# Kernel optimization log

Measured on AMD Instinct MI355X. Metric: run time of the kernel, lower is better.

## Reference

```python
import jax, jax.numpy as jnp
import numpy as np
import math

H = 8  # num_heads

def setup_inputs() -> dict:
    key = jax.random.key(0)
    ks = jax.random.split(key, 12)
    B, N, M, k = 2, 8192, 8192, 32
    dq, dk, dv = 256, 256, 256
    s = 1.0 / math.sqrt(dq)
    inp = {
        'Q': jax.random.normal(ks[0], (B, N, dq), dtype=jnp.float32),
        'K': jax.random.normal(ks[1], (B, M, dk), dtype=jnp.float32),
        'neighbours': jax.random.randint(ks[2], (B, N, k), 0, M),
        'Wq': jax.random.normal(ks[3], (dq, dv), dtype=jnp.float32) * s,
        'bq': jnp.zeros((dv,), dtype=jnp.float32),
        'Wk': jax.random.normal(ks[4], (dk, dv), dtype=jnp.float32) * s,
        'bk': jnp.zeros((dv,), dtype=jnp.float32),
        'Wv': jax.random.normal(ks[5], (dk, dv), dtype=jnp.float32) * s,
        'bv': jnp.zeros((dv,), dtype=jnp.float32),
        'Wo': jax.random.normal(ks[6], (dv, dv), dtype=jnp.float32) * (1.0 / math.sqrt(dv)),
        'bo': jnp.zeros((dv,), dtype=jnp.float32),
    }
    return inp

def reference(Q, K, neighbours, Wq, bq, Wk, bk, Wv, bv, Wo, bo):
    B, N, _ = Q.shape
    dv = Wq.shape[1]
    ds = dv // H
    # project and split heads (contiguous channel chunks == reshape)
    Qh = (Q @ Wq + bq).reshape(B, N, H, ds)            # [B,N,H,ds]
    Kh = (K @ Wk + bk).reshape(B, -1, H, ds)           # [B,M,H,ds]
    Vh = (K @ Wv + bv).reshape(B, -1, H, ds)           # [B,M,H,ds]
    # gather per-node kNN neighbour keys/values: [B,N,k,H,ds]
    gather = jax.vmap(lambda x, idx: x[idx])
    Kn = gather(Kh, neighbours)
    Vn = gather(Vh, neighbours)
    # scale uses full latent size (faithful to original), not head dim
    scale = 1.0 / math.sqrt(dv)
    E = jnp.einsum('bnhd,bnkhd->bnhk', Qh, Kn) * scale  # [B,N,H,k]
    A = jax.nn.softmax(E, axis=-1)
    AV = jnp.einsum('bnhk,bnkhd->bnhd', A, Vn).reshape(B, N, dv)
    return AV @ Wo + bo
```

## Files before the change

### kernel.cpp

```cpp
#include <hip/hip_runtime.h>
#include <stdint.h>

typedef unsigned short u16;
typedef __attribute__((ext_vector_type(8))) short short8;
typedef __attribute__((ext_vector_type(4))) float f32x4;

__device__ __forceinline__ float bf2f(u16 u) {
    union { unsigned int i; float f; } v;
    v.i = ((unsigned int)u) << 16;
    return v.f;
}
__device__ __forceinline__ u16 f2bf(float f) {
    union { float f; unsigned int i; } v; v.f = f;
    unsigned int b = v.i;
    return (u16)((b + 0x7FFFu + ((b >> 16) & 1u)) >> 16);
}

typedef const __attribute__((address_space(1))) void* as1cv;
typedef __attribute__((address_space(3))) void* as3v;
__device__ __forceinline__ void gload16(const void* g, void* l) {
    __builtin_amdgcn_global_load_lds((as1cv)g, (as3v)l, 16, 0, 0);
}

__global__ __launch_bounds__(256) void prep(
    const float* __restrict__ Q, const float* __restrict__ K,
    const float* __restrict__ Wq, const float* __restrict__ Wk,
    const float* __restrict__ Wv, const float* __restrict__ Wo,
    u16* __restrict__ Qb, u16* __restrict__ Kb,
    u16* __restrict__ Tq, u16* __restrict__ Tk,
    u16* __restrict__ Tv, u16* __restrict__ To)
{
    __shared__ u16 ts[64][65];
    int bi = blockIdx.x;
    int t = threadIdx.x;
    if (bi < 4096) {
        const float* src = (bi < 2048) ? Q : K;
        u16* dst = (bi < 2048) ? Qb : Kb;
        int blk = bi & 2047;
        size_t i = ((size_t)blk * 256 + t) * 8;
        float4 a = *reinterpret_cast<const float4*>(src + i);
        float4 b = *reinterpret_cast<const float4*>(src + i + 4);
        u16 o[8] = {f2bf(a.x), f2bf(a.y), f2bf(a.z), f2bf(a.w),
                    f2bf(b.x), f2bf(b.y), f2bf(b.z), f2bf(b.w)};
        *reinterpret_cast<uint4*>(dst + i) = *reinterpret_cast<const uint4*>(o);
        return;
    }
    int wi = bi - 4096;
    int wsel = wi >> 4;
    const float* W = wsel == 0 ? Wq : wsel == 1 ? Wk : wsel == 2 ? Wv : Wo;
    u16*        T  = wsel == 0 ? Tq : wsel == 1 ? Tk : wsel == 2 ? Tv : To;
    int k0 = ((wi >> 2) & 3) * 64, n0 = (wi & 3) * 64;
    int r = t >> 2, cq = (t & 3) * 16;
    const float4* src = reinterpret_cast<const float4*>(W + (k0 + r) * 256 + n0 + cq);
    for (int u = 0; u < 4; ++u) {
        float4 v = src[u];
        int c = cq + u * 4;
        ts[r][c + 0] = f2bf(v.x); ts[r][c + 1] = f2bf(v.y);
        ts[r][c + 2] = f2bf(v.z); ts[r][c + 3] = f2bf(v.w);
    }
    __syncthreads();
    u16* dst = T + (n0 + r) * 256 + k0 + cq;
    for (int u = 0; u < 16; ++u) dst[u] = ts[cq + u][r];
}

__global__ __launch_bounds__(256) void gemm_proj(
    const u16* __restrict__ Qb, const u16* __restrict__ Kb,
    const u16* __restrict__ Wtq, const u16* __restrict__ Wtk, const u16* __restrict__ Wtv,
    const float* __restrict__ bq, const float* __restrict__ bk, const float* __restrict__ bv,
    u16* __restrict__ Qh, u16* __restrict__ Kh, u16* __restrict__ Vh)
{
    int z = blockIdx.z;
    const u16*   Ab   = (z == 0) ? Qb  : Kb;
    const u16*   Wt   = (z == 0) ? Wtq : (z == 1) ? Wtk : Wtv;
    const float* bias = (z == 0) ? bq  : (z == 1) ? bk  : bv;
    u16*         C    = (z == 0) ? Qh  : (z == 1) ? Kh  : Vh;

    __shared__ u16 As[64 * 64];
    __shared__ u16 Bs[128 * 64];

    int t = threadIdx.x;
    int lane = t & 63, w = t >> 6;
    int row0 = blockIdx.x * 64, col0 = blockIdx.y * 128;
    int wr = (w >> 1) * 32, wc = (w & 1) * 64;
    int qd = lane >> 4, md = lane & 15;

    int lrow = lane >> 3;
    int scol = (lane & 7) * 8;

    f32x4 acc[2][4] = {};

    for (int kt = 0; kt < 256; kt += 64) {
#pragma unroll
        for (int u = 0; u < 2; ++u) {
            int ch = w * 2 + u;
            gload16(Ab + (size_t)(row0 + ch * 8 + lrow) * 256 + kt + scol,
                    (char*)As + ch * 1024);
        }
#pragma unroll
        for (int u = 0; u < 4; ++u) {
            int ch = w * 4 + u;
            gload16(Wt + (size_t)(col0 + ch * 8 + lrow) * 256 + kt + scol,
                    (char*)Bs + ch * 1024);
        }
        __syncthreads();
#pragma unroll
        for (int ks = 0; ks < 64; ks += 32) {
            short8 af[2], bf[4];
#pragma unroll
            for (int i = 0; i < 2; ++i)
                af[i] = *reinterpret_cast<const short8*>(
                    &As[(wr + i * 16 + md) * 64 + ks + qd * 8]);
#pragma unroll
            for (int j = 0; j < 4; ++j)
                bf[j] = *reinterpret_cast<const short8*>(
                    &Bs[(wc + j * 16 + md) * 64 + ks + qd * 8]);
#pragma unroll
            for (int i = 0; i < 2; ++i)
#pragma unroll
                for (int j = 0; j < 4; ++j)
                    acc[i][j] = __builtin_amdgcn_mfma_f32_16x16x32_bf16(
                        af[i], bf[j], acc[i][j], 0, 0, 0);
        }
        __syncthreads();
    }

#pragma unroll
    for (int i = 0; i < 2; ++i)
#pragma unroll
        for (int j = 0; j < 4; ++j) {
            int col = col0 + wc + j * 16 + md;
            float b = bias[col];
#pragma unroll
            for (int r = 0; r < 4; ++r) {
                int row = row0 + wr + i * 16 + qd * 4 + r;
                C[(size_t)row * 256 + col] = f2bf(acc[i][j][r] + b);
            }
        }
}

__global__ __launch_bounds__(256) void gemm_out(
    const u16* __restrict__ Ab, const u16* __restrict__ Wt,
    const float* __restrict__ bias, float* __restrict__ Cout)
{
    __shared__ u16 As[64 * 64];
    __shared__ u16 Bs[64 * 64];

    int t = threadIdx.x;
    int lane = t & 63, w = t >> 6;
    int row0 = blockIdx.x * 64, col0 = blockIdx.y * 64;
    int wr = (w >> 1) * 32, wc = (w & 1) * 32;
    int qd = lane >> 4, md = lane & 15;

    int lrow = lane >> 3;
    int scol = (lane & 7) * 8;

    f32x4 acc[2][2] = {};

    for (int kt = 0; kt < 256; kt += 64) {
#pragma unroll
        for (int u = 0; u < 2; ++u) {
            int ch = w * 2 + u;
            gload16(Ab + (size_t)(row0 + ch * 8 + lrow) * 256 + kt + scol,
                    (char*)As + ch * 1024);
            gload16(Wt + (size_t)(col0 + ch * 8 + lrow) * 256 + kt + scol,
                    (char*)Bs + ch * 1024);
        }
        __syncthreads();
#pragma unroll
        for (int ks = 0; ks < 64; ks += 32) {
            short8 af[2], bf[2];
#pragma unroll
            for (int i = 0; i < 2; ++i)
                af[i] = *reinterpret_cast<const short8*>(
                    &As[(wr + i * 16 + md) * 64 + ks + qd * 8]);
#pragma unroll
            for (int j = 0; j < 2; ++j)
                bf[j] = *reinterpret_cast<const short8*>(
                    &Bs[(wc + j * 16 + md) * 64 + ks + qd * 8]);
#pragma unroll
            for (int i = 0; i < 2; ++i)
#pragma unroll
                for (int j = 0; j < 2; ++j)
                    acc[i][j] = __builtin_amdgcn_mfma_f32_16x16x32_bf16(
                        af[i], bf[j], acc[i][j], 0, 0, 0);
        }
        __syncthreads();
    }

#pragma unroll
    for (int i = 0; i < 2; ++i)
#pragma unroll
        for (int j = 0; j < 2; ++j) {
            int col = col0 + wc + j * 16 + md;
            float b = bias[col];
#pragma unroll
            for (int r = 0; r < 4; ++r) {
                int row = row0 + wr + i * 16 + qd * 4 + r;
                Cout[(size_t)row * 256 + col] = acc[i][j][r] + b;
            }
        }
}

__global__ __launch_bounds__(256) void attn(
    const u16* __restrict__ Qh, const u16* __restrict__ Kh, const u16* __restrict__ Vh,
    const int* __restrict__ nbr, u16* __restrict__ AVb)
{
    __shared__ float qs[2][256];
    __shared__ float as_[2][256];
    __shared__ int jb[2][32];

    int t = threadIdx.x;
    int row0 = blockIdx.x * 2;
    int b = row0 >> 13;

    {
        int r = t >> 7, c = (t & 127) * 2;
        unsigned int v = *reinterpret_cast<const unsigned int*>(
            Qh + (size_t)(row0 + r) * 256 + c);
        union { unsigned int i; float f; } lo, hi;
        lo.i = v << 16; hi.i = v & 0xffff0000u;
        qs[r][c] = lo.f; qs[r][c + 1] = hi.f;
    }
    if (t < 64) {
        int r = t >> 5, j = t & 31;
        int ji = nbr[(size_t)(row0 + r) * 32 + j];
        jb[r][j] = ((b << 13) + ji) << 9;
    }
    __syncthreads();

    int h = t >> 5, j = t & 31;
#pragma unroll
    for (int r = 0; r < 2; ++r) {
        const char* kp = (const char*)Kh + jb[r][j] + h * 64;
        uint4 kw[4];
        kw[0] = *reinterpret_cast<const uint4*>(kp);
        kw[1] = *reinterpret_cast<const uint4*>(kp + 16);
        kw[2] = *reinterpret_cast<const uint4*>(kp + 32);
        kw[3] = *reinterpret_cast<const uint4*>(kp + 48);
        const float* q = &qs[r][h * 32];
        float e = 0.f;
#pragma unroll
        for (int cq4 = 0; cq4 < 4; ++cq4) {
            unsigned int wds[4] = {kw[cq4].x, kw[cq4].y, kw[cq4].z, kw[cq4].w};
#pragma unroll
            for (int u = 0; u < 4; ++u) {
                union { unsigned int i; float f; } lo, hi;
                lo.i = wds[u] << 16; hi.i = wds[u] & 0xffff0000u;
                e += q[cq4 * 8 + u * 2] * lo.f + q[cq4 * 8 + u * 2 + 1] * hi.f;
            }
        }
        e *= 0.0625f;
        float m = e;
        for (int off = 16; off; off >>= 1) m = fmaxf(m, __shfl_xor(m, off, 32));
        float p = __expf(e - m);
        float s = p;
        for (int off = 16; off; off >>= 1) s += __shfl_xor(s, off, 32);
        as_[r][t] = p / s;
    }
    __syncthreads();

    {
        int r = t >> 7, c = t & 127, hh = c >> 4;
        const float* aw = &as_[r][hh * 32];
        float a0 = 0.f, a1 = 0.f;
#pragma unroll
        for (int jj = 0; jj < 32; ++jj) {
            unsigned int v = *reinterpret_cast<const unsigned int*>(
                (const char*)Vh + jb[r][jj] + c * 4);
            union { unsigned int i; float f; } lo, hi;
            lo.i = v << 16; hi.i = v & 0xffff0000u;
            float wgt = aw[jj];
            a0 += wgt * lo.f; a1 += wgt * hi.f;
        }
        u16 o[2] = {f2bf(a0), f2bf(a1)};
        *reinterpret_cast<unsigned int*>(AVb + (size_t)(row0 + r) * 256 + c * 2) =
            *reinterpret_cast<const unsigned int*>(o);
    }
}

extern "C" void kernel_launch(void* const* d_in, const int* in_sizes, int n_in,
                              void* d_out, int out_size, void* d_ws, size_t ws_size,
                              hipStream_t stream) {
    const float* Q   = (const float*)d_in[0];
    const float* K   = (const float*)d_in[1];
    const int*   nbr = (const int*)d_in[2];
    const float* Wq  = (const float*)d_in[3];
    const float* bq  = (const float*)d_in[4];
    const float* Wk  = (const float*)d_in[5];
    const float* bk  = (const float*)d_in[6];
    const float* Wv  = (const float*)d_in[7];
    const float* bv  = (const float*)d_in[8];
    const float* Wo  = (const float*)d_in[9];
    const float* bo  = (const float*)d_in[10];
    float* out = (float*)d_out;

    char* ws = (char*)d_ws;
    size_t off = 0;
    auto alloc = [&](size_t bytes) -> void* {
        void* p = ws + off;
        off += (bytes + 255) & ~(size_t)255;
        return p;
    };
    const size_t MN = 16384;
    u16* Wtq = (u16*)alloc(256 * 256 * 2);
    u16* Wtk = (u16*)alloc(256 * 256 * 2);
    u16* Wtv = (u16*)alloc(256 * 256 * 2);
    u16* Wto = (u16*)alloc(256 * 256 * 2);
    u16* Qb  = (u16*)alloc(MN * 256 * 2);
    u16* Kb  = (u16*)alloc(MN * 256 * 2);
    u16* Qh  = (u16*)alloc(MN * 256 * 2);
    u16* Kh  = (u16*)alloc(MN * 256 * 2);
    u16* Vh  = (u16*)alloc(MN * 256 * 2);
    u16* AVb = (u16*)alloc(MN * 256 * 2);

    prep<<<dim3(4160), 256, 0, stream>>>(Q, K, Wq, Wk, Wv, Wo,
                                         Qb, Kb, Wtq, Wtk, Wtv, Wto);
    gemm_proj<<<dim3(256, 2, 3), 256, 0, stream>>>(Qb, Kb, Wtq, Wtk, Wtv,
                                                   bq, bk, bv, Qh, Kh, Vh);
    attn<<<dim3(8192), 256, 0, stream>>>(Qh, Kh, Vh, nbr, AVb);
    gemm_out<<<dim3(256, 4), 256, 0, stream>>>(AVb, Wto, bo, out);
}
```

Baseline: 170.8 us.

## Fuse fp32-to-bf16 input conversion into projection GEMM and retile kernels

Removes the separate Q/K fp32-to-bf16 conversion pass. The projection GEMM now loads fp32 tiles directly into LDS with an XOR swizzle and converts them to bf16 in registers, using 128x128 tiles. The output GEMM moves to 64x128 tiles with swizzled LDS, and the attention kernel handles 4 rows per block, using vectorized V loads and readfirstlane offsets. This cuts a full HBM round trip for Q and K, at the cost of larger LDS use (48KB) and more conversion work inside the GEMM loop.

```diff
diff --git a/kernel.cpp b/kernel.cpp
--- a/kernel.cpp
+++ b/kernel.cpp
@@ -1,55 +1,43 @@
 #include <hip/hip_runtime.h>
+#include <hip/hip_bf16.h>
 #include <stdint.h>
 
 typedef unsigned short u16;
 typedef __attribute__((ext_vector_type(8))) short short8;
 typedef __attribute__((ext_vector_type(4))) float f32x4;
 
-__device__ __forceinline__ float bf2f(u16 u) {
-    union { unsigned int i; float f; } v;
-    v.i = ((unsigned int)u) << 16;
-    return v.f;
-}
 __device__ __forceinline__ u16 f2bf(float f) {
     union { float f; unsigned int i; } v; v.f = f;
     unsigned int b = v.i;
     return (u16)((b + 0x7FFFu + ((b >> 16) & 1u)) >> 16);
 }
 
+__device__ __forceinline__ short8 cvt8(float4 a, float4 b) {
+    union { __hip_bfloat162 h[4]; short8 s; } u;
+    u.h[0] = __float22bfloat162_rn(make_float2(a.x, a.y));
+    u.h[1] = __float22bfloat162_rn(make_float2(a.z, a.w));
+    u.h[2] = __float22bfloat162_rn(make_float2(b.x, b.y));
+    u.h[3] = __float22bfloat162_rn(make_float2(b.z, b.w));
+    return u.s;
+}
+
 typedef const __attribute__((address_space(1))) void* as1cv;
 typedef __attribute__((address_space(3))) void* as3v;
 __device__ __forceinline__ void gload16(const void* g, void* l) {
     __builtin_amdgcn_global_load_lds((as1cv)g, (as3v)l, 16, 0, 0);
 }
 
-__global__ __launch_bounds__(256) void prep(
-    const float* __restrict__ Q, const float* __restrict__ K,
-    const float* __restrict__ Wq, const float* __restrict__ Wk,
-    const float* __restrict__ Wv, const float* __restrict__ Wo,
-    u16* __restrict__ Qb, u16* __restrict__ Kb,
-    u16* __restrict__ Tq, u16* __restrict__ Tk,
-    u16* __restrict__ Tv, u16* __restrict__ To)
+__global__ __launch_bounds__(256) void wprep(
+    const float* __restrict__ W0, const float* __restrict__ W1,
+    const float* __restrict__ W2, const float* __restrict__ W3,
+    u16* __restrict__ T0, u16* __restrict__ T1,
+    u16* __restrict__ T2, u16* __restrict__ T3)
 {
+    const float* W = blockIdx.z == 0 ? W0 : blockIdx.z == 1 ? W1 : blockIdx.z == 2 ? W2 : W3;
+    u16*        T  = blockIdx.z == 0 ? T0 : blockIdx.z == 1 ? T1 : blockIdx.z == 2 ? T2 : T3;
     __shared__ u16 ts[64][65];
-    int bi = blockIdx.x;
+    int k0 = blockIdx.x * 64, n0 = blockIdx.y * 64;
     int t = threadIdx.x;
-    if (bi < 4096) {
-        const float* src = (bi < 2048) ? Q : K;
-        u16* dst = (bi < 2048) ? Qb : Kb;
-        int blk = bi & 2047;
-        size_t i = ((size_t)blk * 256 + t) * 8;
-        float4 a = *reinterpret_cast<const float4*>(src + i);
-        float4 b = *reinterpret_cast<const float4*>(src + i + 4);
-        u16 o[8] = {f2bf(a.x), f2bf(a.y), f2bf(a.z), f2bf(a.w),
-                    f2bf(b.x), f2bf(b.y), f2bf(b.z), f2bf(b.w)};
-        *reinterpret_cast<uint4*>(dst + i) = *reinterpret_cast<const uint4*>(o);
-        return;
-    }
-    int wi = bi - 4096;
-    int wsel = wi >> 4;
-    const float* W = wsel == 0 ? Wq : wsel == 1 ? Wk : wsel == 2 ? Wv : Wo;
-    u16*        T  = wsel == 0 ? Tq : wsel == 1 ? Tk : wsel == 2 ? Tv : To;
-    int k0 = ((wi >> 2) & 3) * 64, n0 = (wi & 3) * 64;
     int r = t >> 2, cq = (t & 3) * 16;
     const float4* src = reinterpret_cast<const float4*>(W + (k0 + r) * 256 + n0 + cq);
     for (int u = 0; u < 4; ++u) {
@@ -64,17 +52,92 @@
 }
 
 __global__ __launch_bounds__(256) void gemm_proj(
-    const u16* __restrict__ Qb, const u16* __restrict__ Kb,
+    const float* __restrict__ Q, const float* __restrict__ K,
     const u16* __restrict__ Wtq, const u16* __restrict__ Wtk, const u16* __restrict__ Wtv,
     const float* __restrict__ bq, const float* __restrict__ bk, const float* __restrict__ bv,
     u16* __restrict__ Qh, u16* __restrict__ Kh, u16* __restrict__ Vh)
 {
     int z = blockIdx.z;
-    const u16*   Ab   = (z == 0) ? Qb  : Kb;
+    const float* Af   = (z == 0) ? Q   : K;
     const u16*   Wt   = (z == 0) ? Wtq : (z == 1) ? Wtk : Wtv;
     const float* bias = (z == 0) ? bq  : (z == 1) ? bk  : bv;
     u16*         C    = (z == 0) ? Qh  : (z == 1) ? Kh  : Vh;
 
+    __shared__ float Asf[128 * 64];
+    __shared__ u16   Bs[128 * 64];
+
+    int t = threadIdx.x;
+    int lane = t & 63, w = t >> 6;
+    int row0 = blockIdx.x * 128, col0 = blockIdx.y * 128;
+    int wr = (w >> 1) * 64, wc = (w & 1) * 64;
+    int qd = lane >> 4, md = lane & 15;
+
+    f32x4 acc[4][4] = {};
+
+    for (int kt = 0; kt < 256; kt += 64) {
+#pragma unroll
+        for (int u = 0; u < 8; ++u) {
+            int chunk = w * 8 + u;
+            int s = chunk * 64 + lane;
+            int r = s >> 4, c = s & 15;
+            gload16(Af + (size_t)(row0 + r) * 256 + kt + ((c ^ (r & 15)) * 4),
+                    (char*)Asf + chunk * 1024);
+        }
+#pragma unroll
+        for (int u = 0; u < 4; ++u) {
+            int chunk = w * 4 + u;
+            int s = chunk * 64 + lane;
+            int r = s >> 3, c = s & 7;
+            gload16(Wt + (size_t)(col0 + r) * 256 + kt + ((c ^ (r & 7)) * 8),
+                    (char*)Bs + chunk * 1024);
+        }
+        __syncthreads();
+#pragma unroll
+        for (int ks = 0; ks < 64; ks += 32) {
+            short8 af[4], bf[4];
+#pragma unroll
+            for (int i = 0; i < 4; ++i) {
+                int ar = wr + i * 16 + md;
+                int c0 = (ks >> 2) + qd * 2;
+                int x = ar & 15;
+                float4 fa0 = reinterpret_cast<const float4*>(Asf)[ar * 16 + (c0 ^ x)];
+                float4 fa1 = reinterpret_cast<const float4*>(Asf)[ar * 16 + ((c0 + 1) ^ x)];
+                af[i] = cvt8(fa0, fa1);
+            }
+#pragma unroll
+            for (int j = 0; j < 4; ++j) {
+                int br = wc + j * 16 + md;
+                int slot = ((ks >> 3) + qd) ^ (br & 7);
+                bf[j] = reinterpret_cast<const short8*>(Bs)[br * 8 + slot];
+            }
+#pragma unroll
+            for (int i = 0; i < 4; ++i)
+#pragma unroll
+                for (int j = 0; j < 4; ++j)
+                    acc[i][j] = __builtin_amdgcn_mfma_f32_16x16x32_bf16(
+                        af[i], bf[j], acc[i][j], 0, 0, 0);
+        }
+        __syncthreads();
+    }
+
+#pragma unroll
+    for (int i = 0; i < 4; ++i)
+#pragma unroll
+        for (int j = 0; j < 4; ++j) {
+            int col = col0 + wc + j * 16 + md;
+            float b = bias[col];
+#pragma unroll
+            for (int r = 0; r < 4; ++r) {
+                int row = row0 + wr + i * 16 + qd * 4 + r;
+                C[(size_t)row * 256 + col] = f2bf(acc[i][j][r] + b);
+            }
+        }
+}
+
+__global__ __launch_bounds__(256) void gemm_out(
+    const u16* __restrict__ Ab, const u16* __restrict__ Wt,
+    const float* __restrict__ bias, float* __restrict__ Cout)
+{
     __shared__ u16 As[64 * 64];
     __shared__ u16 Bs[128 * 64];
 
@@ -84,36 +147,41 @@
     int wr = (w >> 1) * 32, wc = (w & 1) * 64;
     int qd = lane >> 4, md = lane & 15;
 
-    int lrow = lane >> 3;
-    int scol = (lane & 7) * 8;
-
     f32x4 acc[2][4] = {};
 
     for (int kt = 0; kt < 256; kt += 64) {
 #pragma unroll
         for (int u = 0; u < 2; ++u) {
-            int ch = w * 2 + u;
-            gload16(Ab + (size_t)(row0 + ch * 8 + lrow) * 256 + kt + scol,
-                    (char*)As + ch * 1024);
+            int chunk = w * 2 + u;
+            int s = chunk * 64 + lane;
+            int r = s >> 3, c = s & 7;
+            gload16(Ab + (size_t)(row0 + r) * 256 + kt + ((c ^ (r & 7)) * 8),
+                    (char*)As + chunk * 1024);
         }
 #pragma unroll
         for (int u = 0; u < 4; ++u) {
-            int ch = w * 4 + u;
-            gload16(Wt + (size_t)(col0 + ch * 8 + lrow) * 256 + kt + scol,
-                    (char*)Bs + ch * 1024);
+            int chunk = w * 4 + u;
+            int s = chunk * 64 + lane;
+            int r = s >> 3, c = s & 7;
+            gload16(Wt + (size_t)(col0 + r) * 256 + kt + ((c ^ (r & 7)) * 8),
+                    (char*)Bs + chunk * 1024);
         }
         __syncthreads();
 #pragma unroll
         for (int ks = 0; ks < 64; ks += 32) {
             short8 af[2], bf[4];
 #pragma unroll
-            for (int i = 0; i < 2; ++i)
-                af[i] = *reinterpret_cast<const short8*>(
-                    &As[(wr + i * 16 + md) * 64 + ks + qd * 8]);
-#pragma unroll
-            for (int j = 0; j < 4; ++j)
-                bf[j] = *reinterpret_cast<const short8*>(
-                    &Bs[(wc + j * 16 + md) * 64 + ks + qd * 8]);
+            for (int i = 0; i < 2; ++i) {
+                int ar = wr + i * 16 + md;
+                int slot = ((ks >> 3) + qd) ^ (ar & 7);
+                af[i] = reinterpret_cast<const short8*>(As)[ar * 8 + slot];
+            }
+#pragma unroll
+            for (int j = 0; j < 4; ++j) {
+                int br = wc + j * 16 + md;
+                int slot = ((ks >> 3) + qd) ^ (br & 7);
+                bf[j] = reinterpret_cast<const short8*>(Bs)[br * 8 + slot];
+            }
 #pragma unroll
             for (int i = 0; i < 2; ++i)
 #pragma unroll
@@ -128,69 +196,6 @@
     for (int i = 0; i < 2; ++i)
 #pragma unroll
         for (int j = 0; j < 4; ++j) {
-            int col = col0 + wc + j * 16 + md;
-            float b = bias[col];
-#pragma unroll
-            for (int r = 0; r < 4; ++r) {
-                int row = row0 + wr + i * 16 + qd * 4 + r;
-                C[(size_t)row * 256 + col] = f2bf(acc[i][j][r] + b);
-            }
-        }
-}
-
-__global__ __launch_bounds__(256) void gemm_out(
-    const u16* __restrict__ Ab, const u16* __restrict__ Wt,
-    const float* __restrict__ bias, float* __restrict__ Cout)
-{
-    __shared__ u16 As[64 * 64];
-    __shared__ u16 Bs[64 * 64];
-
-    int t = threadIdx.x;
-    int lane = t & 63, w = t >> 6;
-    int row0 = blockIdx.x * 64, col0 = blockIdx.y * 64;
-    int wr = (w >> 1) * 32, wc = (w & 1) * 32;
-    int qd = lane >> 4, md = lane & 15;
-
-    int lrow = lane >> 3;
-    int scol = (lane & 7) * 8;
-
-    f32x4 acc[2][2] = {};
-
-    for (int kt = 0; kt < 256; kt += 64) {
-#pragma unroll
-        for (int u = 0; u < 2; ++u) {
-            int ch = w * 2 + u;
-            gload16(Ab + (size_t)(row0 + ch * 8 + lrow) * 256 + kt + scol,
-                    (char*)As + ch * 1024);
-            gload16(Wt + (size_t)(col0 + ch * 8 + lrow) * 256 + kt + scol,
-                    (char*)Bs + ch * 1024);
-        }
-        __syncthreads();
-#pragma unroll
-        for (int ks = 0; ks < 64; ks += 32) {
-            short8 af[2], bf[2];
-#pragma unroll
-            for (int i = 0; i < 2; ++i)
-                af[i] = *reinterpret_cast<const short8*>(
-                    &As[(wr + i * 16 + md) * 64 + ks + qd * 8]);
-#pragma unroll
-            for (int j = 0; j < 2; ++j)
-                bf[j] = *reinterpret_cast<const short8*>(
-                    &Bs[(wc + j * 16 + md) * 64 + ks + qd * 8]);
-#pragma unroll
-            for (int i = 0; i < 2; ++i)
-#pragma unroll
-                for (int j = 0; j < 2; ++j)
-                    acc[i][j] = __builtin_amdgcn_mfma_f32_16x16x32_bf16(
-                        af[i], bf[j], acc[i][j], 0, 0, 0);
-        }
-        __syncthreads();
-    }
-
-#pragma unroll
-    for (int i = 0; i < 2; ++i)
-#pragma unroll
-        for (int j = 0; j < 2; ++j) {
             int col = col0 + wc + j * 16 + md;
             float b = bias[col];
 #pragma unroll
@@ -205,23 +210,25 @@
     const u16* __restrict__ Qh, const u16* __restrict__ Kh, const u16* __restrict__ Vh,
     const int* __restrict__ nbr, u16* __restrict__ AVb)
 {
-    __shared__ float qs[2][256];
-    __shared__ float as_[2][256];
-    __shared__ int jb[2][32];
+    __shared__ float qs[4][256];
+    __shared__ float as_[4][256];
+    __shared__ int jb[4][32];
 
     int t = threadIdx.x;
-    int row0 = blockIdx.x * 2;
+    int row0 = blockIdx.x * 4;
     int b = row0 >> 13;
 
-    {
-        int r = t >> 7, c = (t & 127) * 2;
+#pragma unroll
+    for (int rr = 0; rr < 2; ++rr) {
+        int idx = rr * 256 + t;
+        int r = idx >> 7, c = (idx & 127) * 2;
         unsigned int v = *reinterpret_cast<const unsigned int*>(
             Qh + (size_t)(row0 + r) * 256 + c);
         union { unsigned int i; float f; } lo, hi;
         lo.i = v << 16; hi.i = v & 0xffff0000u;
         qs[r][c] = lo.f; qs[r][c + 1] = hi.f;
     }
-    if (t < 64) {
+    if (t < 128) {
         int r = t >> 5, j = t & 31;
         int ji = nbr[(size_t)(row0 + r) * 32 + j];
         jb[r][j] = ((b << 13) + ji) << 9;
@@ -230,7 +237,7 @@
 
     int h = t >> 5, j = t & 31;
 #pragma unroll
-    for (int r = 0; r < 2; ++r) {
+    for (int r = 0; r < 4; ++r) {
         const char* kp = (const char*)Kh + jb[r][j] + h * 64;
         uint4 kw[4];
         kw[0] = *reinterpret_cast<const uint4*>(kp);
@@ -260,21 +267,29 @@
     __syncthreads();
 
     {
-        int r = t >> 7, c = t & 127, hh = c >> 4;
-        const float* aw = &as_[r][hh * 32];
-        float a0 = 0.f, a1 = 0.f;
+        int r = t >> 6, c2 = t & 63;
+        int hh = c2 >> 3;
+        float wv[32];
+#pragma unroll
+        for (int u = 0; u < 8; ++u)
+            *reinterpret_cast<float4*>(&wv[u * 4]) =
+                *reinterpret_cast<const float4*>(&as_[r][hh * 32 + u * 4]);
+        float a0 = 0.f, a1 = 0.f, a2 = 0.f, a3 = 0.f;
 #pragma unroll
         for (int jj = 0; jj < 32; ++jj) {
-            unsigned int v = *reinterpret_cast<const unsigned int*>(
-                (const char*)Vh + jb[r][jj] + c * 4);
-            union { unsigned int i; float f; } lo, hi;
-            lo.i = v << 16; hi.i = v & 0xffff0000u;
-            float wgt = aw[jj];
-            a0 += wgt * lo.f; a1 += wgt * hi.f;
-        }
-        u16 o[2] = {f2bf(a0), f2bf(a1)};
-        *reinterpret_cast<unsigned int*>(AVb + (size_t)(row0 + r) * 256 + c * 2) =
-            *reinterpret_cast<const unsigned int*>(o);
+            int off = __builtin_amdgcn_readfirstlane(jb[r][jj]);
+            uint2 v = *reinterpret_cast<const uint2*>(
+                (const char*)Vh + off + c2 * 8);
+            union { unsigned int i; float f; } l0, h0, l1, h1;
+            l0.i = v.x << 16; h0.i = v.x & 0xffff0000u;
+            l1.i = v.y << 16; h1.i = v.y & 0xffff0000u;
+            float wgt = wv[jj];
+            a0 += wgt * l0.f; a1 += wgt * h0.f;
+            a2 += wgt * l1.f; a3 += wgt * h1.f;
+        }
+        u16 o[4] = {f2bf(a0), f2bf(a1), f2bf(a2), f2bf(a3)};
+        *reinterpret_cast<uint2*>(AVb + (size_t)(row0 + r) * 256 + c2 * 4) =
+            *reinterpret_cast<const uint2*>(o);
     }
 }
 
@@ -306,17 +321,14 @@
     u16* Wtk = (u16*)alloc(256 * 256 * 2);
     u16* Wtv = (u16*)alloc(256 * 256 * 2);
     u16* Wto = (u16*)alloc(256 * 256 * 2);
-    u16* Qb  = (u16*)alloc(MN * 256 * 2);
-    u16* Kb  = (u16*)alloc(MN * 256 * 2);
     u16* Qh  = (u16*)alloc(MN * 256 * 2);
     u16* Kh  = (u16*)alloc(MN * 256 * 2);
     u16* Vh  = (u16*)alloc(MN * 256 * 2);
     u16* AVb = (u16*)alloc(MN * 256 * 2);
 
-    prep<<<dim3(4160), 256, 0, stream>>>(Q, K, Wq, Wk, Wv, Wo,
-                                         Qb, Kb, Wtq, Wtk, Wtv, Wto);
-    gemm_proj<<<dim3(256, 2, 3), 256, 0, stream>>>(Qb, Kb, Wtq, Wtk, Wtv,
+    wprep<<<dim3(4, 4, 4), 256, 0, stream>>>(Wq, Wk, Wv, Wo, Wtq, Wtk, Wtv, Wto);
+    gemm_proj<<<dim3(128, 2, 3), 256, 0, stream>>>(Q, K, Wtq, Wtk, Wtv,
                                                    bq, bk, bv, Qh, Kh, Vh);
-    attn<<<dim3(8192), 256, 0, stream>>>(Qh, Kh, Vh, nbr, AVb);
-    gemm_out<<<dim3(256, 4), 256, 0, stream>>>(AVb, Wto, bo, out);
-}
+    attn<<<dim3(4096), 256, 0, stream>>>(Qh, Kh, Vh, nbr, AVb);
+    gemm_out<<<dim3(256, 2), 256, 0, stream>>>(AVb, Wto, bo, out);
+}
```

After: 171.0 us. No clear change (+0.1%).
